# Kernel tuning notes

Hardware: AMD Instinct MI355X
Metric: run time of the kernel (lower is better)

## Reference

```python
import jax, jax.numpy as jnp
import numpy as np

S = 32          # input grid resolution
N = 2048        # active input voxels
C = 256         # in channels
CO = 128        # out channels
S2 = 2 * S      # upsampled resolution
M = 8 * N       # candidate child voxels
EPS = 1e-6


def setup_inputs() -> dict:
    key = jax.random.key(0)
    ks = jax.random.split(key, 8)
    # unique voxel coordinates (sparse occupancy)
    lin = jax.random.permutation(ks[0], S ** 3)[:N]
    coords = jnp.stack([lin // (S * S), (lin // S) % S, lin % S], axis=-1).astype(jnp.int32)
    sc = 0.05
    return {
        "feats": jax.random.normal(ks[1], (N, C), jnp.float32),
        "norm1_w": 1.0 + 0.1 * jax.random.normal(ks[2], (C,), jnp.float32),
        "norm1_b": 0.1 * jax.random.normal(ks[3], (C,), jnp.float32),
        "subdiv_w": sc * jax.random.normal(ks[4], (C, 8), jnp.float32),
        "subdiv_b": jnp.zeros((8,), jnp.float32),
        "conv1_w": sc * jax.random.normal(ks[5], (27, C, CO), jnp.float32),
        "conv1_b": jnp.zeros((CO,), jnp.float32),
        "conv2_w": sc * jax.random.normal(ks[6], (27, CO, CO), jnp.float32),
        "conv2_b": jnp.zeros((CO,), jnp.float32),
        "skip_w": sc * jax.random.normal(ks[7], (C, CO), jnp.float32),
        "skip_b": jnp.zeros((CO,), jnp.float32),
        "coords": coords,
    }


def _layernorm(x, w=None, b=None):
    # LayerNorm32: fp32 math, eps=1e-6
    m = jnp.mean(x, axis=-1, keepdims=True)
    v = jnp.var(x, axis=-1, keepdims=True)
    y = (x - m) * jax.lax.rsqrt(v + EPS)
    if w is not None:
        y = y * w + b
    return y


def _sparse_conv(feats, nidx, w, b):
    # submanifold 3x3x3 sparse conv: gather 27 neighbors, contract.
    # nidx: [M,27] with sentinel M pointing at a zero row.
    pad = jnp.concatenate([feats, jnp.zeros((1, feats.shape[1]), feats.dtype)], axis=0)
    g = pad[nidx]                                   # [M, 27, Cin]
    return jnp.einsum('nkc,kcd->nd', g, w) + b


def _forward(feats, norm1_w, norm1_b, subdiv_w, subdiv_b, conv1_w, conv1_b,
             conv2_w, conv2_b, skip_w, skip_b, coords):
    # subdiv prediction (SparseLinear C -> 8)
    subdiv = feats @ subdiv_w + subdiv_b            # [N, 8]
    # norm1 + silu
    h = jax.nn.silu(_layernorm(feats, norm1_w, norm1_b))
    # sparse upsample x2 with octree subdivision mask
    mask = (subdiv > 0).reshape(-1)                 # [M]
    j = jnp.arange(8, dtype=jnp.int32)
    offs8 = jnp.stack([(j >> 2) & 1, (j >> 1) & 1, j & 1], axis=-1)  # [8,3]
    cc = (coords[:, None, :] * 2 + offs8[None]).reshape(-1, 3)        # [M,3]
    h_c = jnp.where(mask[:, None], jnp.repeat(h, 8, axis=0), 0.0)     # [M,C]
    x_c = jnp.where(mask[:, None], jnp.repeat(feats, 8, axis=0), 0.0)
    # neighbor lookup grid (padded by 1; default M -> zero feature row)
    grid = jnp.full((S2 + 2, S2 + 2, S2 + 2), M, jnp.int32)
    grid = grid.at[cc[:, 0] + 1, cc[:, 1] + 1, cc[:, 2] + 1].set(
        jnp.arange(M, dtype=jnp.int32))
    d = jnp.arange(-1, 2, dtype=jnp.int32)
    offs27 = jnp.stack(jnp.meshgrid(d, d, d, indexing='ij'), axis=-1).reshape(27, 3)
    nc = cc[:, None, :] + 1 + offs27[None]          # [M,27,3]
    nidx = grid[nc[..., 0], nc[..., 1], nc[..., 2]] # [M,27]
    # conv1 -> norm2 (no affine) -> silu -> conv2
    h1 = jax.nn.silu(_layernorm(_sparse_conv(h_c, nidx, conv1_w, conv1_b)))
    h2 = _sparse_conv(h1, nidx, conv2_w, conv2_b)
    # residual with linear skip; mask out non-subdivided children
    out = (h2 + x_c @ skip_w + skip_b) * mask[:, None].astype(h2.dtype)
    return out, subdiv


def reference(feats, norm1_w, norm1_b, subdiv_w, subdiv_b, conv1_w, conv1_b,
              conv2_w, conv2_b, skip_w, skip_b, coords):
    return _forward(feats, norm1_w, norm1_b, subdiv_w, subdiv_b, conv1_w,
                    conv1_b, conv2_w, conv2_b, skip_w, skip_b, coords)
```

## Files before the change

### kernel.cpp

```cpp
#include <hip/hip_runtime.h>
#include <cstdint>
#include <cstddef>

constexpr int N  = 2048;
constexpr int C  = 256;
constexpr int CO = 128;
constexpr int M  = 16384;
constexpr int G  = 66;
constexpr int KP = 7;
constexpr int KCHUNK = 4;
constexpr float EPS = 1e-6f;

using bf8 = __attribute__((ext_vector_type(8))) short;
using f4  = __attribute__((ext_vector_type(4))) float;

static __device__ __forceinline__ unsigned short f2bf(float f) {
  unsigned u = __float_as_uint(f);
  u += 0x7fffu + ((u >> 16) & 1u);
  return (unsigned short)(u >> 16);
}
static __device__ __forceinline__ float bf2f(unsigned short s) {
  return __uint_as_float((unsigned)s << 16);
}

__global__ __launch_bounds__(256) void k_prep(
    const float* __restrict__ c1w, unsigned short* __restrict__ w1t,
    const float* __restrict__ c2w, unsigned short* __restrict__ w2t,
    int* __restrict__ grid, unsigned short* __restrict__ h,
    unsigned short* __restrict__ h1) {
  int i = blockIdx.x * 256 + threadIdx.x;
  if (i < G * G * G) grid[i] = M;
  if (blockIdx.x == 1200) {
    if (threadIdx.x < C) h[(size_t)N * C + threadIdx.x] = 0;
  }
  if (blockIdx.x == 1201) {
    if (threadIdx.x < CO) h1[(size_t)M * CO + threadIdx.x] = 0;
  }

  __shared__ float tile[32][33];
  int bx = blockIdx.x;
  const float* w; unsigned short* wtp; int cin, k, cb, ob;
  if (bx < 864) {
    w = c1w; wtp = w1t; cin = C;
    k = bx >> 5; int tl = bx & 31; cb = tl >> 2; ob = tl & 3;
  } else {
    int b2 = bx - 864;
    w = c2w; wtp = w2t; cin = CO;
    k = b2 >> 4; int tl = b2 & 15; cb = tl >> 2; ob = tl & 3;
  }
  int ty = threadIdx.x >> 5, tx = threadIdx.x & 31;
#pragma unroll
  for (int j = 0; j < 4; ++j) {
    int row = ty + j * 8;
    tile[row][tx] = w[((size_t)k * cin + cb * 32 + row) * CO + ob * 32 + tx];
  }
  __syncthreads();
#pragma unroll
  for (int j = 0; j < 4; ++j) {
    int row = ty + j * 8;
    wtp[((size_t)k * CO + ob * 32 + row) * cin + cb * 32 + tx] =
        f2bf(tile[tx][row]);
  }
}

__global__ __launch_bounds__(256) void k_rownorm(
    const float* __restrict__ feats, const float* __restrict__ n1w,
    const float* __restrict__ n1b, const float* __restrict__ sdw,
    const float* __restrict__ sdb, float* __restrict__ out_subdiv,
    unsigned short* __restrict__ h, int* __restrict__ pidx,
    float* __restrict__ maskf, const int* __restrict__ coords,
    int* __restrict__ grid, const float* __restrict__ skw,
    const float* __restrict__ skb, float* __restrict__ sres) {
  int n = blockIdx.x, t = threadIdx.x;
  __shared__ float sx[256];
  __shared__ float sacc[256];
  float x = feats[(size_t)n * C + t];
  sx[t] = x;
  float4 w0 = *(const float4*)(sdw + t * 8);
  float4 w1 = *(const float4*)(sdw + t * 8 + 4);
  float v[10] = {x * w0.x, x * w0.y, x * w0.z, x * w0.w,
                 x * w1.x, x * w1.y, x * w1.z, x * w1.w, x, x * x};
#pragma unroll
  for (int mk = 1; mk < 64; mk <<= 1) {
#pragma unroll
    for (int j = 0; j < 10; ++j) v[j] += __shfl_xor(v[j], mk, 64);
  }
  __shared__ float red[4][10];
  int wave = t >> 6, lane = t & 63;
  if (lane == 0) {
#pragma unroll
    for (int j = 0; j < 10; ++j) red[wave][j] = v[j];
  }
  __syncthreads();
  float sums[10];
#pragma unroll
  for (int j = 0; j < 10; ++j)
    sums[j] = red[0][j] + red[1][j] + red[2][j] + red[3][j];
  float mean = sums[8] / (float)C;
  float var  = sums[9] / (float)C - mean * mean;
  float rstd = rsqrtf(var + EPS);
  if (t < 8) {
    float sd = sums[t] + sdb[t];
    out_subdiv[(size_t)n * 8 + t] = sd;
    bool mk = sd > 0.f;
    pidx[n * 8 + t]  = mk ? n : N;
    maskf[n * 8 + t] = mk ? 1.f : 0.f;
    int xx = coords[n * 3 + 0] * 2 + ((t >> 2) & 1) + 1;
    int yy = coords[n * 3 + 1] * 2 + ((t >> 1) & 1) + 1;
    int zz = coords[n * 3 + 2] * 2 + (t & 1) + 1;
    grid[(xx * G + yy) * G + zz] = n * 8 + t;
  }
  float y  = (x - mean) * rstd * n1w[t] + n1b[t];
  float sl = y / (1.f + __expf(-y));
  h[(size_t)n * C + t] = f2bf(sl);

  int o = t & 127, half = t >> 7;
  const float* wp = skw + (size_t)(half * 128) * CO + o;
  const float* xs = sx + half * 128;
  float a = 0.f;
#pragma unroll 8
  for (int c = 0; c < 128; ++c) a += xs[c] * wp[(size_t)c * CO];
  sacc[t] = a;
  __syncthreads();
  if (t < 128) sres[(size_t)n * CO + t] = sacc[t] + sacc[t + 128] + skb[t];
}

__global__ void k_nidx(const int* __restrict__ coords, const int* __restrict__ grid,
                       const int* __restrict__ pidx, int* __restrict__ nidxt,
                       int* __restrict__ g1t) {
  int idx = blockIdx.x * 256 + threadIdx.x;
  if (idx >= M * 27) return;
  int m = idx & (M - 1);
  int k = idx >> 14;
  int p = m >> 3, j = m & 7;
  int dx = k / 9 - 1;
  int dy = (k / 3) % 3 - 1;
  int dz = k % 3 - 1;
  int x = coords[p * 3 + 0] * 2 + ((j >> 2) & 1) + 1 + dx;
  int y = coords[p * 3 + 1] * 2 + ((j >> 1) & 1) + 1 + dy;
  int z = coords[p * 3 + 2] * 2 + (j & 1) + 1 + dz;
  int gv = grid[(x * G + y) * G + z];
  nidxt[idx] = gv;
  g1t[idx] = (gv == M) ? N : pidx[gv];
}

template <int CIN, int NCB>
__global__ __launch_bounds__(256, 3) void k_conv(
    const unsigned short* __restrict__ src, const int* __restrict__ gt,
    const unsigned short* __restrict__ wt, unsigned short* __restrict__ part) {
  __shared__ unsigned short sB[2][128 * 32];
  const int t = threadIdx.x;
  const int w = t >> 6, lane = t & 63;
  const int quad = lane >> 4, ln = lane & 15;
  const int m0 = blockIdx.x * 128;
  const int kpart = blockIdx.y;
  const int k0 = kpart * KCHUNK;
  const int nk = min(KCHUNK, 27 - k0);
  const int nstage = nk * NCB;
  const int rh = (w >> 1) * 64, ch = (w & 1) * 64;

  const int row2 = t >> 1;
  const int c0 = (t & 1) * 2;
  const int x3 = (row2 >> 1) & 3;
  const int wsl0 = row2 * 32 + ((c0) ^ x3) * 8;
  const int wsl1 = row2 * 32 + ((c0 + 1) ^ x3) * 8;
  const int slot = (quad ^ ((ln >> 1) & 3)) * 8;

  const int* gbase = gt + (size_t)k0 * M + m0 + rh + ln;

  bf8 rb0, rb1;
  bf8 ra[4], rn[4];
  int ga[4], gn[4];

  auto loadB = [&](int s) {
    const int kk = s / NCB, cb = s - kk * NCB;
    const unsigned short* pb =
        wt + ((size_t)(k0 + kk) * CO + row2) * CIN + cb * 32 + c0 * 8;
    rb0 = *(const bf8*)(pb);
    rb1 = *(const bf8*)(pb + 8);
  };
  auto writeB = [&](int buf) {
    *(bf8*)(sB[buf] + wsl0) = rb0;
    *(bf8*)(sB[buf] + wsl1) = rb1;
  };

  f4 acc[16];
  f4 zero = {0.f, 0.f, 0.f, 0.f};
#pragma unroll
  for (int i = 0; i < 16; ++i) acc[i] = zero;

#pragma unroll
  for (int ti = 0; ti < 4; ++ti) ga[ti] = gbase[ti * 16];
  loadB(0);
#pragma unroll
  for (int ti = 0; ti < 4; ++ti)
    ra[ti] = *(const bf8*)(src + (size_t)ga[ti] * CIN + quad * 8);
  writeB(0);

  for (int s = 0; s < nstage; ++s) {
    const int buf = s & 1;
    const int kk = s / NCB, cb = s - kk * NCB;
    const bool have = (s + 1 < nstage);
    if (cb == 0 && kk + 1 < nk) {
#pragma unroll
      for (int ti = 0; ti < 4; ++ti) gn[ti] = gbase[(size_t)(kk + 1) * M + ti * 16];
    }
    if (have) {
      loadB(s + 1);
      const int cb1 = (cb + 1 < NCB) ? cb + 1 : 0;
      const int* gu = (cb + 1 < NCB) ? ga : gn;
#pragma unroll
      for (int ti = 0; ti < 4; ++ti)
        rn[ti] = *(const bf8*)(src + (size_t)gu[ti] * CIN + cb1 * 32 + quad * 8);
    }
    __syncthreads();
    const unsigned short* pb = sB[buf];
    bf8 bv[4];
#pragma unroll
    for (int tj = 0; tj < 4; ++tj)
      bv[tj] = *(const bf8*)(pb + (ch + tj * 16 + ln) * 32 + slot);
#pragma unroll
    for (int ti = 0; ti < 4; ++ti)
#pragma unroll
      for (int tj = 0; tj < 4; ++tj)
        acc[ti * 4 + tj] = __builtin_amdgcn_mfma_f32_16x16x32_bf16(
            ra[ti], bv[tj], acc[ti * 4 + tj], 0, 0, 0);
    if (have) {
      writeB(buf ^ 1);
#pragma unroll
      for (int ti = 0; ti < 4; ++ti) ra[ti] = rn[ti];
      if (cb + 1 == NCB) {
#pragma unroll
        for (int ti = 0; ti < 4; ++ti) ga[ti] = gn[ti];
      }
    }
  }

  unsigned short* pp = part + ((size_t)kpart * M + m0) * CO;
#pragma unroll
  for (int ti = 0; ti < 4; ++ti) {
    int mrow = rh + ti * 16 + quad * 4;
#pragma unroll
    for (int tj = 0; tj < 4; ++tj) {
      int co = ch + tj * 16 + ln;
#pragma unroll
      for (int rr = 0; rr < 4; ++rr)
        pp[(size_t)(mrow + rr) * CO + co] = f2bf(acc[ti * 4 + tj][rr]);
    }
  }
}

__global__ __launch_bounds__(256) void k_r1(const unsigned short* __restrict__ p,
                                            const float* __restrict__ bias,
                                            unsigned short* __restrict__ h1) {
  int wave = threadIdx.x >> 6, lane = threadIdx.x & 63;
  int m = blockIdx.x * 4 + wave;
  float v0 = bias[lane], v1 = bias[lane + 64];
#pragma unroll
  for (int q = 0; q < KP; ++q) {
    const unsigned short* pq = p + ((size_t)q * M + m) * CO;
    v0 += bf2f(pq[lane]);
    v1 += bf2f(pq[lane + 64]);
  }
  float sum = v0 + v1, sq = v0 * v0 + v1 * v1;
#pragma unroll
  for (int mk = 1; mk < 64; mk <<= 1) {
    sum += __shfl_xor(sum, mk, 64);
    sq  += __shfl_xor(sq, mk, 64);
  }
  float mean = sum / (float)CO;
  float var  = sq / (float)CO - mean * mean;
  float rstd = rsqrtf(var + EPS);
  float y0 = (v0 - mean) * rstd;
  float y1 = (v1 - mean) * rstd;
  float s0 = y0 / (1.f + __expf(-y0));
  float s1 = y1 / (1.f + __expf(-y1));
  h1[(size_t)m * CO + lane]      = f2bf(s0);
  h1[(size_t)m * CO + lane + 64] = f2bf(s1);
}

__global__ __launch_bounds__(256) void k_r2(const unsigned short* __restrict__ p,
                                            const float* __restrict__ bias,
                                            const float* __restrict__ sres,
                                            const float* __restrict__ maskf,
                                            float* __restrict__ out) {
  int i = blockIdx.x * 256 + threadIdx.x;
  int m = i >> 5;
  int o4 = (i & 31) * 4;
  float4 acc = *(const float4*)(bias + o4);
#pragma unroll
  for (int q = 0; q < KP; ++q) {
    ushort4 a = *(const ushort4*)(p + ((size_t)q * M + m) * CO + o4);
    acc.x += bf2f(a.x); acc.y += bf2f(a.y);
    acc.z += bf2f(a.z); acc.w += bf2f(a.w);
  }
  float4 s = *(const float4*)(sres + (size_t)(m >> 3) * CO + o4);
  float mk = maskf[m];
  float4 r;
  r.x = (acc.x + s.x) * mk;
  r.y = (acc.y + s.y) * mk;
  r.z = (acc.z + s.z) * mk;
  r.w = (acc.w + s.w) * mk;
  *(float4*)(out + (size_t)m * CO + o4) = r;
}

extern "C" void kernel_launch(void* const* d_in, const int* in_sizes, int n_in,
                              void* d_out, int out_size, void* d_ws, size_t ws_size,
                              hipStream_t stream) {
  const float* feats = (const float*)d_in[0];
  const float* n1w   = (const float*)d_in[1];
  const float* n1b   = (const float*)d_in[2];
  const float* sdw   = (const float*)d_in[3];
  const float* sdb   = (const float*)d_in[4];
  const float* c1w   = (const float*)d_in[5];
  const float* c1b   = (const float*)d_in[6];
  const float* c2w   = (const float*)d_in[7];
  const float* c2b   = (const float*)d_in[8];
  const float* skw   = (const float*)d_in[9];
  const float* skb   = (const float*)d_in[10];
  const int* coords  = (const int*)d_in[11];
  float* out = (float*)d_out;

  char* ws = (char*)d_ws;
  size_t off = 0;
  auto alloc = [&](size_t bytes) -> char* {
    char* p = ws + off;
    off += (bytes + 255) & ~(size_t)255;
    return p;
  };
  unsigned short* h    = (unsigned short*)alloc((size_t)(N + 1) * C * 2);
  unsigned short* h1   = (unsigned short*)alloc((size_t)(M + 1) * CO * 2);
  int*   grid  = (int*)alloc((size_t)G * G * G * 4);
  int*   nidxt = (int*)alloc((size_t)27 * M * 4);
  int*   g1t   = (int*)alloc((size_t)27 * M * 4);
  int*   pidx  = (int*)alloc((size_t)M * 4);
  float* maskf = (float*)alloc((size_t)M * 4);
  float* sres  = (float*)alloc((size_t)N * CO * 4);
  unsigned short* w1t = (unsigned short*)alloc((size_t)27 * CO * C * 2);
  unsigned short* w2t = (unsigned short*)alloc((size_t)27 * CO * CO * 2);
  unsigned short* pc  = (unsigned short*)alloc((size_t)KP * M * CO * 2);

  k_prep<<<1296, 256, 0, stream>>>(c1w, w1t, c2w, w2t, grid, h, h1);
  k_rownorm<<<N, 256, 0, stream>>>(feats, n1w, n1b, sdw, sdb,
                                   out + (size_t)M * CO, h, pidx, maskf,
                                   coords, grid, skw, skb, sres);
  k_nidx<<<(M * 27 + 255) / 256, 256, 0, stream>>>(coords, grid, pidx, nidxt, g1t);

  k_conv<C, 8><<<dim3(M / 128, KP), 256, 0, stream>>>(h, g1t, w1t, pc);
  k_r1<<<M / 4, 256, 0, stream>>>(pc, c1b, h1);

  k_conv<CO, 4><<<dim3(M / 128, KP), 256, 0, stream>>>(h1, nidxt, w2t, pc);
  k_r2<<<M * CO / 4 / 256, 256, 0, stream>>>(pc, c2b, sres, maskf, out);
}
```

Measured before the change: 202.8 us.

## Fuse neighbor index lookup into conv kernels and rebalance tap split

Removes the separate neighbor-index kernel and its two 27*M index tables. Each conv block now computes its voxels' grid base offsets from the coordinates and looks up every tap's neighbor directly in the dense grid, mapping through pidx for the first conv. The tap split also changes from 7 chunks of 4 to 6 chunks of 5, which cuts partial-sum traffic but gives fewer blocks. The trade-off is extra dependent grid and pidx loads inside the conv pipeline, which could add latency.

```diff
diff --git a/kernel.cpp b/kernel.cpp
--- a/kernel.cpp
+++ b/kernel.cpp
@@ -7,8 +7,8 @@
 constexpr int CO = 128;
 constexpr int M  = 16384;
 constexpr int G  = 66;
-constexpr int KP = 7;
-constexpr int KCHUNK = 4;
+constexpr int KP = 6;
+constexpr int KCHUNK = 5;
 constexpr float EPS = 1e-6f;
 
 using bf8 = __attribute__((ext_vector_type(8))) short;
@@ -125,28 +125,10 @@
   if (t < 128) sres[(size_t)n * CO + t] = sacc[t] + sacc[t + 128] + skb[t];
 }
 
-__global__ void k_nidx(const int* __restrict__ coords, const int* __restrict__ grid,
-                       const int* __restrict__ pidx, int* __restrict__ nidxt,
-                       int* __restrict__ g1t) {
-  int idx = blockIdx.x * 256 + threadIdx.x;
-  if (idx >= M * 27) return;
-  int m = idx & (M - 1);
-  int k = idx >> 14;
-  int p = m >> 3, j = m & 7;
-  int dx = k / 9 - 1;
-  int dy = (k / 3) % 3 - 1;
-  int dz = k % 3 - 1;
-  int x = coords[p * 3 + 0] * 2 + ((j >> 2) & 1) + 1 + dx;
-  int y = coords[p * 3 + 1] * 2 + ((j >> 1) & 1) + 1 + dy;
-  int z = coords[p * 3 + 2] * 2 + (j & 1) + 1 + dz;
-  int gv = grid[(x * G + y) * G + z];
-  nidxt[idx] = gv;
-  g1t[idx] = (gv == M) ? N : pidx[gv];
-}
-
-template <int CIN, int NCB>
+template <int CIN, int NCB, bool UP>
 __global__ __launch_bounds__(256, 3) void k_conv(
-    const unsigned short* __restrict__ src, const int* __restrict__ gt,
+    const unsigned short* __restrict__ src, const int* __restrict__ coords,
+    const int* __restrict__ grid, const int* __restrict__ pidx,
     const unsigned short* __restrict__ wt, unsigned short* __restrict__ part) {
   __shared__ unsigned short sB[2][128 * 32];
   const int t = threadIdx.x;
@@ -166,7 +148,24 @@
   const int wsl1 = row2 * 32 + ((c0 + 1) ^ x3) * 8;
   const int slot = (quad ^ ((ln >> 1) & 3)) * 8;
 
-  const int* gbase = gt + (size_t)k0 * M + m0 + rh + ln;
+  int gb[4];
+#pragma unroll
+  for (int ti = 0; ti < 4; ++ti) {
+    int m = m0 + rh + ti * 16 + ln;
+    int p = m >> 3, j = m & 7;
+    int cx = coords[p * 3 + 0] * 2 + ((j >> 2) & 1) + 1;
+    int cy = coords[p * 3 + 1] * 2 + ((j >> 1) & 1) + 1;
+    int cz = coords[p * 3 + 2] * 2 + (j & 1) + 1;
+    gb[ti] = (cx * G + cy) * G + cz;
+  }
+  auto tapoff = [&](int k) {
+    return (k / 9 - 1) * (G * G) + ((k / 3) % 3 - 1) * G + (k % 3 - 1);
+  };
+  auto lookup = [&](int ti, int doff) {
+    int g = grid[gb[ti] + doff];
+    if (UP) return (g >= M) ? N : pidx[g & (M - 1)];
+    return g;
+  };
 
   bf8 rb0, rb1;
   bf8 ra[4], rn[4];
@@ -189,8 +188,11 @@
 #pragma unroll
   for (int i = 0; i < 16; ++i) acc[i] = zero;
 
-#pragma unroll
-  for (int ti = 0; ti < 4; ++ti) ga[ti] = gbase[ti * 16];
+  {
+    int d0 = tapoff(k0);
+#pragma unroll
+    for (int ti = 0; ti < 4; ++ti) ga[ti] = lookup(ti, d0);
+  }
   loadB(0);
 #pragma unroll
   for (int ti = 0; ti < 4; ++ti)
@@ -202,8 +204,9 @@
     const int kk = s / NCB, cb = s - kk * NCB;
     const bool have = (s + 1 < nstage);
     if (cb == 0 && kk + 1 < nk) {
-#pragma unroll
-      for (int ti = 0; ti < 4; ++ti) gn[ti] = gbase[(size_t)(kk + 1) * M + ti * 16];
+      int dn = tapoff(k0 + kk + 1);
+#pragma unroll
+      for (int ti = 0; ti < 4; ++ti) gn[ti] = lookup(ti, dn);
     }
     if (have) {
       loadB(s + 1);
@@ -331,8 +334,6 @@
   unsigned short* h    = (unsigned short*)alloc((size_t)(N + 1) * C * 2);
   unsigned short* h1   = (unsigned short*)alloc((size_t)(M + 1) * CO * 2);
   int*   grid  = (int*)alloc((size_t)G * G * G * 4);
-  int*   nidxt = (int*)alloc((size_t)27 * M * 4);
-  int*   g1t   = (int*)alloc((size_t)27 * M * 4);
   int*   pidx  = (int*)alloc((size_t)M * 4);
   float* maskf = (float*)alloc((size_t)M * 4);
   float* sres  = (float*)alloc((size_t)N * CO * 4);
@@ -344,11 +345,12 @@
   k_rownorm<<<N, 256, 0, stream>>>(feats, n1w, n1b, sdw, sdb,
                                    out + (size_t)M * CO, h, pidx, maskf,
                                    coords, grid, skw, skb, sres);
-  k_nidx<<<(M * 27 + 255) / 256, 256, 0, stream>>>(coords, grid, pidx, nidxt, g1t);
-
-  k_conv<C, 8><<<dim3(M / 128, KP), 256, 0, stream>>>(h, g1t, w1t, pc);
+
+  k_conv<C, 8, true><<<dim3(M / 128, KP), 256, 0, stream>>>(h, coords, grid,
+                                                            pidx, w1t, pc);
   k_r1<<<M / 4, 256, 0, stream>>>(pc, c1b, h1);
 
-  k_conv<CO, 4><<<dim3(M / 128, KP), 256, 0, stream>>>(h1, nidxt, w2t, pc);
+  k_conv<CO, 4, false><<<dim3(M / 128, KP), 256, 0, stream>>>(h1, coords, grid,
+                                                              pidx, w2t, pc);
   k_r2<<<M * CO / 4 / 256, 256, 0, stream>>>(pc, c2b, sres, maskf, out);
 }
```

Result: faster. 193.8 us (-4.4%).
